# Kernel tuning notes

Hardware: AMD Instinct MI355X
Metric: run time of the kernel (lower is better)

The kernel has to match this reference:

```python
import jax, jax.numpy as jnp
import numpy as np

H = 16        # num_heads
D_HEAD = 128  # head_dim
D = H * D_HEAD  # hidden_size = 2048


def setup_inputs() -> dict:
    key = jax.random.key(0)
    ks = jax.random.split(key, 9)
    s = 1.0 / np.sqrt(D)
    x = jax.random.normal(ks[0], (2, 2048, D), dtype=jnp.float32)
    Wq = jax.random.uniform(ks[1], (D, D), jnp.float32, -s, s)
    bq = jax.random.uniform(ks[2], (D,), jnp.float32, -s, s)
    Wk = jax.random.uniform(ks[3], (D, D), jnp.float32, -s, s)
    bk = jax.random.uniform(ks[4], (D,), jnp.float32, -s, s)
    Wv = jax.random.uniform(ks[5], (D, D), jnp.float32, -s, s)
    bv = jax.random.uniform(ks[6], (D,), jnp.float32, -s, s)
    Wo = jax.random.uniform(ks[7], (D, D), jnp.float32, -s, s)
    bo = jax.random.uniform(ks[8], (D,), jnp.float32, -s, s)
    return {"x": x, "Wq": Wq, "bq": bq, "Wk": Wk, "bk": bk,
            "Wv": Wv, "bv": bv, "Wo": Wo, "bo": bo}


def reference(x, Wq, bq, Wk, bk, Wv, bv, Wo, bo):
    B, T, _ = x.shape
    # Linear projections (torch Linear: x @ W.T + b)
    Q = x @ Wq.T + bq
    K = x @ Wk.T + bk
    V = x @ Wv.T + bv
    # [B, T, H, Dh] -> [B, H, T, Dh]
    Q = Q.reshape(B, T, H, D_HEAD).transpose(0, 2, 1, 3)
    K = K.reshape(B, T, H, D_HEAD).transpose(0, 2, 1, 3)
    V = V.reshape(B, T, H, D_HEAD).transpose(0, 2, 1, 3)
    scores = jnp.einsum('bhqd,bhkd->bhqk', Q, K) / jnp.sqrt(jnp.float32(D_HEAD))
    causal = jnp.tril(jnp.ones((T, T), dtype=bool))
    scores = jnp.where(causal, scores, -jnp.inf)
    probs = jax.nn.softmax(scores, axis=-1)
    ctx = jnp.einsum('bhqk,bhkd->bhqd', probs, V)  # [B, H, T, Dh]
    merged = ctx.transpose(0, 2, 1, 3).reshape(B, T, D)
    return merged @ Wo.T + bo
```

## Files before the change

### kernel.cpp

```cpp
#include <hip/hip_runtime.h>
#include <hip/hip_bf16.h>
#include <math.h>

typedef unsigned short ushort_t;
typedef short bf16x8 __attribute__((ext_vector_type(8)));
typedef float f32x4 __attribute__((ext_vector_type(4)));
typedef float f32x16 __attribute__((ext_vector_type(16)));

#define NH 16
#define DH 128
#define DM 2048
#define TSEQ 2048
#define BT 4096

__device__ __forceinline__ void async16(const void* g, void* l) {
  __builtin_amdgcn_global_load_lds(
      (const __attribute__((address_space(1))) void*)g,
      (__attribute__((address_space(3))) void*)l, 16, 0, 0);
}

__device__ __forceinline__ f32x4 mfma16(bf16x8 a, bf16x8 b, f32x4 c) {
  return __builtin_amdgcn_mfma_f32_16x16x32_bf16(a, b, c, 0, 0, 0);
}
__device__ __forceinline__ f32x16 mfma32(bf16x8 a, bf16x8 b, f32x16 c) {
  return __builtin_amdgcn_mfma_f32_32x32x16_bf16(a, b, c, 0, 0, 0);
}

__device__ __forceinline__ ushort_t f2bf(float f) {
  __hip_bfloat16 h = __float2bfloat16(f);
  return *reinterpret_cast<ushort_t*>(&h);
}
__device__ __forceinline__ unsigned cvtpk_bf16(float lo, float hi_) {
  unsigned r;
  asm("v_cvt_pk_bf16_f32 %0, %1, %2" : "=v"(r) : "v"(lo), "v"(hi_));
  return r;
}
__device__ __forceinline__ float fexp2(float x) {
  float r; asm("v_exp_f32 %0, %1" : "=v"(r) : "v"(x)); return r;
}

__global__ void cvt_all_kernel(const float* __restrict__ x,
                               const float* __restrict__ Wq, const float* __restrict__ Wk,
                               const float* __restrict__ Wv, const float* __restrict__ Wo,
                               ushort_t* __restrict__ xb,
                               ushort_t* __restrict__ Wqb, ushort_t* __restrict__ Wkb,
                               ushort_t* __restrict__ Wvb, ushort_t* __restrict__ Wob)
{
  const int i = blockIdx.x * blockDim.x + threadIdx.x;
  const float* src; ushort_t* dst; int off;
  if (i < (1 << 21)) {
    src = x; dst = xb; off = i;
  } else {
    const int j = i - (1 << 21);
    const int w = j >> 20;
    off = j & ((1 << 20) - 1);
    src = (w == 0) ? Wq : (w == 1) ? Wk : (w == 2) ? Wv : Wo;
    dst = (w == 0) ? Wqb : (w == 1) ? Wkb : (w == 2) ? Wvb : Wob;
  }
  const float4 v = reinterpret_cast<const float4*>(src)[off];
  ushort4 u;
  u.x = f2bf(v.x); u.y = f2bf(v.y); u.z = f2bf(v.z); u.w = f2bf(v.w);
  reinterpret_cast<ushort4*>(dst)[off] = u;
}

__device__ __forceinline__ void stage_half_g(const ushort_t* __restrict__ src,
                                             int row0, int k0,
                                             ushort_t* dst, int tid) {
#pragma unroll
  for (int i = 0; i < 2; ++i) {
    const int idx = i * 512 + tid;
    const int r = idx >> 3, ch = idx & 7;
    const int c = (ch ^ (r & 7)) * 8;
    async16(src + (size_t)(row0 + r) * DM + k0 + c, dst + idx * 8);
  }
}

__global__ __launch_bounds__(512, 2)
void gemm_qkv_fused(const ushort_t* __restrict__ A,
                    const ushort_t* __restrict__ W_0, const ushort_t* __restrict__ W_1,
                    const ushort_t* __restrict__ W_2,
                    const float* __restrict__ b_0, const float* __restrict__ b_1,
                    const float* __restrict__ b_2,
                    ushort_t* __restrict__ outQ, ushort_t* __restrict__ outK,
                    ushort_t* __restrict__ outVt)
{
  constexpr int NK = DM / 64;
  __shared__ __attribute__((aligned(16))) ushort_t As[2][128 * 64];
  __shared__ __attribute__((aligned(16))) ushort_t Bs[2][3][128 * 64];

  const int n0 = blockIdx.x * 128;
  const int m0 = blockIdx.y * 128;
  const int tid = threadIdx.x;
  const int w = tid >> 6, l = tid & 63;
  const int wr = w >> 2, wc = w & 3;
  const int l15 = l & 15, l4 = l >> 4;

  f32x4 acc[3][4][2] = {};
  bf16x8 afr[4][2], bfr[2][2];

  stage_half_g(A,   m0, 0, As[0],    tid);
  stage_half_g(W_0, n0, 0, Bs[0][0], tid);
  stage_half_g(W_1, n0, 0, Bs[0][1], tid);
  stage_half_g(W_2, n0, 0, Bs[0][2], tid);

  for (int kt = 0; kt < NK; ++kt) {
    const int cur = kt & 1;
    if (kt + 1 < NK) {
      const int k1 = (kt + 1) * 64;
      stage_half_g(A,   m0, k1, As[cur ^ 1],    tid);
      stage_half_g(W_0, n0, k1, Bs[cur ^ 1][0], tid);
      stage_half_g(W_1, n0, k1, Bs[cur ^ 1][1], tid);
      stage_half_g(W_2, n0, k1, Bs[cur ^ 1][2], tid);
      asm volatile("s_waitcnt vmcnt(8)" ::: "memory");
    } else {
      asm volatile("s_waitcnt vmcnt(0)" ::: "memory");
    }
    __builtin_amdgcn_s_barrier();

    {
      const char* p_ = reinterpret_cast<const char*>(As[cur]);
#pragma unroll
      for (int mf = 0; mf < 4; ++mf) {
        const int row_ = wr * 64 + mf * 16 + l15;
#pragma unroll
        for (int ks = 0; ks < 2; ++ks)
          afr[mf][ks] = *reinterpret_cast<const bf16x8*>(
              p_ + row_ * 128 + ((l4 * 16 + ks * 64) ^ ((row_ & 7) << 4)));
      }
    }
#pragma unroll
    for (int z = 0; z < 3; ++z) {
      const char* p_ = reinterpret_cast<const char*>(Bs[cur][z]);
#pragma unroll
      for (int nf = 0; nf < 2; ++nf) {
        const int row_ = wc * 32 + nf * 16 + l15;
#pragma unroll
        for (int ks = 0; ks < 2; ++ks)
          bfr[nf][ks] = *reinterpret_cast<const bf16x8*>(
              p_ + row_ * 128 + ((l4 * 16 + ks * 64) ^ ((row_ & 7) << 4)));
      }
      __builtin_amdgcn_s_setprio(1);
#pragma unroll
      for (int mf = 0; mf < 4; ++mf)
#pragma unroll
        for (int nf = 0; nf < 2; ++nf)
#pragma unroll
          for (int ks = 0; ks < 2; ++ks)
            acc[z][mf][nf] = mfma16(afr[mf][ks], bfr[nf][ks], acc[z][mf][nf]);
      __builtin_amdgcn_s_setprio(0);
    }
    asm volatile("" ::: "memory");
    __builtin_amdgcn_s_barrier();
  }

#pragma unroll
  for (int z = 0; z < 3; ++z) {
    const float* bias = (z == 0) ? b_0 : (z == 1) ? b_1 : b_2;
#pragma unroll
    for (int nf = 0; nf < 2; ++nf) {
      const int n = n0 + wc * 32 + nf * 16 + l15;
      const float bv = bias[n];
      const int hh = n >> 7, d = n & 127;
#pragma unroll
      for (int mf = 0; mf < 4; ++mf) {
#pragma unroll
        for (int r = 0; r < 4; ++r) {
          const int m = m0 + wr * 64 + mf * 16 + l4 * 4 + r;
          const float v = acc[z][mf][nf][r] + bv;
          const int b = m >> 11, t = m & 2047;
          const ushort_t val = f2bf(v);
          if (z == 2) {
            outVt[((size_t)(b * NH + hh) * DH + d) * TSEQ + t] = val;
          } else {
            ushort_t* dst = (z == 0) ? outQ : outK;
            dst[((size_t)(b * NH + hh) * TSEQ + t) * DH + d] = val;
          }
        }
      }
    }
  }
}

__device__ __forceinline__ void stage_ab(const ushort_t* __restrict__ A,
                                         const ushort_t* __restrict__ Wp,
                                         int m0, int n0, int k0,
                                         ushort_t* AsB, ushort_t* BsB,
                                         int w, int l)
{
#pragma unroll
  for (int i = 0; i < 4; ++i) {
    const int rb = (i * 4 + w) * 8;
    const int r = rb + (l >> 3);
    const int c = ((l & 7) * 8) ^ ((r & 7) * 8);
    async16(A  + (size_t)(m0 + r) * DM + k0 + c, AsB + rb * 64);
    async16(Wp + (size_t)(n0 + r) * DM + k0 + c, BsB + rb * 64);
  }
}

__global__ __launch_bounds__(256)
void gemm_proj_kernel(const ushort_t* __restrict__ A, const ushort_t* __restrict__ W_0,
                      const float* __restrict__ b_0, float* __restrict__ outF)
{
  constexpr int NK = DM / 64;
  __shared__ __attribute__((aligned(16))) ushort_t As[2][128 * 64];
  __shared__ __attribute__((aligned(16))) ushort_t Bs[2][128 * 64];

  const int n0 = blockIdx.x * 128;
  const int m0 = blockIdx.y * 128;
  const int tid = threadIdx.x;
  const int w = tid >> 6, l = tid & 63;
  const int wm = w >> 1, wn = w & 1;
  const int l15 = l & 15, l4 = l >> 4;

  f32x4 zero = {0.f, 0.f, 0.f, 0.f};
  f32x4 acc[4][4];
#pragma unroll
  for (int i = 0; i < 4; ++i)
#pragma unroll
    for (int j = 0; j < 4; ++j) acc[i][j] = zero;

  stage_ab(A, W_0, m0, n0, 0, As[0], Bs[0], w, l);

  for (int kt = 0; kt < NK; ++kt) {
    const int cur = kt & 1;
    if (kt + 1 < NK) {
      stage_ab(A, W_0, m0, n0, (kt + 1) * 64, As[cur ^ 1], Bs[cur ^ 1], w, l);
      asm volatile("s_waitcnt vmcnt(8)" ::: "memory");
    } else {
      asm volatile("s_waitcnt vmcnt(0)" ::: "memory");
    }
    __builtin_amdgcn_s_barrier();

#pragma unroll
    for (int ks = 0; ks < 2; ++ks) {
      bf16x8 af[4], bfr[4];
#pragma unroll
      for (int mf = 0; mf < 4; ++mf) {
        const int row = wm * 64 + mf * 16 + l15;
        const int byte_ = row * 128 + ((l4 * 16 + ks * 64) ^ ((row & 7) << 4));
        af[mf] = *reinterpret_cast<const bf16x8*>(reinterpret_cast<const char*>(As[cur]) + byte_);
      }
#pragma unroll
      for (int nf = 0; nf < 4; ++nf) {
        const int row = wn * 64 + nf * 16 + l15;
        const int byte_ = row * 128 + ((l4 * 16 + ks * 64) ^ ((row & 7) << 4));
        bfr[nf] = *reinterpret_cast<const bf16x8*>(reinterpret_cast<const char*>(Bs[cur]) + byte_);
      }
      __builtin_amdgcn_s_setprio(1);
#pragma unroll
      for (int mf = 0; mf < 4; ++mf)
#pragma unroll
        for (int nf = 0; nf < 4; ++nf)
          acc[mf][nf] = mfma16(af[mf], bfr[nf], acc[mf][nf]);
      __builtin_amdgcn_s_setprio(0);
    }
    asm volatile("" ::: "memory");
    __builtin_amdgcn_s_barrier();
  }

#pragma unroll
  for (int nf = 0; nf < 4; ++nf) {
    const int n = n0 + wn * 64 + nf * 16 + l15;
    const float bv = b_0[n];
#pragma unroll
    for (int mf = 0; mf < 4; ++mf) {
#pragma unroll
      for (int r = 0; r < 4; ++r) {
        const int m = m0 + wm * 64 + mf * 16 + l4 * 4 + r;
        outF[(size_t)m * DM + n] = acc[mf][nf][r] + bv;
      }
    }
  }
}

__device__ __forceinline__ void stage_kv(const ushort_t* __restrict__ Kg,
                                         const ushort_t* __restrict__ Vt,
                                         size_t kbase, size_t vbase, int kv0,
                                         ushort_t* KsB, ushort_t* VsB, int tid)
{
#pragma unroll
  for (int i = 0; i < 4; ++i) {
    const int idx = i * 256 + tid;
    const int r = idx >> 4, ch = idx & 15;
    const int c = (ch ^ (r & 7)) * 8;
    async16(Kg + kbase + (size_t)(kv0 + r) * DH + c, KsB + idx * 8);
  }
#pragma unroll
  for (int i = 0; i < 4; ++i) {
    const int idx = i * 256 + tid;
    const int d = idx >> 3, ch = idx & 7;
    const int c = (ch ^ (d & 7)) * 8;
    async16(Vt + vbase + (size_t)d * TSEQ + kv0 + c, VsB + idx * 8);
  }
}

__global__ __launch_bounds__(256)
void attn_kernel(const ushort_t* __restrict__ Q, const ushort_t* __restrict__ Kg,
                 const ushort_t* __restrict__ Vt, ushort_t* __restrict__ ctx)
{
  __shared__ __attribute__((aligned(16))) ushort_t Ks[2][64 * 128];
  __shared__ __attribute__((aligned(16))) ushort_t Vs[2][128 * 64];

  const int fid = (int)blockIdx.x + 16 * (int)blockIdx.y;
  const int xcd = fid & 7;
  const int s   = fid >> 3;
  const int bh  = xcd * 4 + (s & 3);
  const int qt  = (s < 32) ? (15 - (s >> 2)) : ((s - 32) >> 2);

  const int tid = threadIdx.x, w = tid >> 6, l = tid & 63;
  const int l31 = l & 31, hi = l >> 5;
  const size_t kbase = (size_t)bh * TSEQ * DH;
  const size_t vbase = (size_t)bh * DH * TSEQ;
  const int bq0 = qt * 128;
  const int wq0 = bq0 + w * 32;
  const int NT = qt * 2 + 2;
  const int q = wq0 + l31;
  const float C2 = 0.12753842f;
  const float NEG = -3.0e38f;

  bf16x8 aq[8];
  {
    const ushort_t* qp = Q + kbase + (size_t)q * DH + hi * 8;
#pragma unroll
    for (int st = 0; st < 8; ++st)
      aq[st] = *reinterpret_cast<const bf16x8*>(qp + st * 16);
  }

  f32x16 o[4] = {};
  float m_r = NEG, l_r = 0.f;

  stage_kv(Kg, Vt, kbase, vbase, 0, Ks[0], Vs[0], tid);

  for (int kt = 0; kt < NT; ++kt) {
    const int kv0 = kt * 64, cur = kt & 1;
    if (kt + 1 < NT) {
      stage_kv(Kg, Vt, kbase, vbase, kv0 + 64, Ks[cur ^ 1], Vs[cur ^ 1], tid);
      asm volatile("s_waitcnt vmcnt(8)" ::: "memory");
    } else {
      asm volatile("s_waitcnt vmcnt(0)" ::: "memory");
    }
    __builtin_amdgcn_s_barrier();

    if (kv0 <= wq0 + 31) {
      const char* ksb = reinterpret_cast<const char*>(Ks[cur]);
      f32x16 s0 = {}, s1 = {};
      __builtin_amdgcn_s_setprio(1);
#pragma unroll
      for (int st = 0; st < 8; ++st) {
        const int byt = l31 * 256 + ((hi * 16 + st * 32) ^ ((l31 & 7) << 4));
        bf16x8 ak0 = *reinterpret_cast<const bf16x8*>(ksb + byt);
        bf16x8 ak1 = *reinterpret_cast<const bf16x8*>(ksb + byt + 8192);
        s0 = mfma32(ak0, aq[st], s0);
        s1 = mfma32(ak1, aq[st], s1);
      }
      __builtin_amdgcn_s_setprio(0);

      if (kv0 + 63 > wq0) {
#pragma unroll
        for (int r = 0; r < 16; ++r) {
          const int kvl = kv0 + (r & 3) + 8 * (r >> 2) + 4 * hi;
          if (kvl > q)      s0[r] = NEG;
          if (kvl + 32 > q) s1[r] = NEG;
        }
      }

      float t8[8];
#pragma unroll
      for (int r = 0; r < 8; ++r)
        t8[r] = fmaxf(fmaxf(s0[r], s0[r + 8]), fmaxf(s1[r], s1[r + 8]));
#pragma unroll
      for (int r = 0; r < 4; ++r) t8[r] = fmaxf(t8[r], t8[r + 4]);
      float mt = fmaxf(fmaxf(t8[0], t8[1]), fmaxf(t8[2], t8[3]));
      mt = fmaxf(mt, __shfl_xor(mt, 32));

      const float mnew = fmaxf(m_r, mt);
      if (!__all(mt <= m_r + 16.0f)) {
        const float alpha = fexp2((m_r - mnew) * C2);
        l_r *= alpha;
#pragma unroll
        for (int d0 = 0; d0 < 4; ++d0) o[d0] *= alpha;
        m_r = mnew;
      }

#pragma unroll
      for (int r = 0; r < 16; ++r) {
        s0[r] = fexp2((s0[r] - m_r) * C2);
        s1[r] = fexp2((s1[r] - m_r) * C2);
      }
      float sm[8];
#pragma unroll
      for (int r = 0; r < 8; ++r) sm[r] = (s0[r] + s0[r + 8]) + (s1[r] + s1[r + 8]);
#pragma unroll
      for (int r = 0; r < 4; ++r) sm[r] += sm[r + 4];
      float ls = (sm[0] + sm[1]) + (sm[2] + sm[3]);
      ls += __shfl_xor(ls, 32);
      l_r += ls;

      const char* vsb = reinterpret_cast<const char*>(Vs[cur]);
#pragma unroll
      for (int ks = 0; ks < 4; ++ks) {
        float pj[8];
#pragma unroll
        for (int j = 0; j < 8; ++j)
          pj[j] = (ks >> 1) ? s1[(ks & 1) * 8 + j] : s0[(ks & 1) * 8 + j];
        unsigned cA = cvtpk_bf16(pj[0], pj[1]);
        unsigned cB = cvtpk_bf16(pj[2], pj[3]);
        unsigned cC = cvtpk_bf16(pj[4], pj[5]);
        unsigned cD = cvtpk_bf16(pj[6], pj[7]);
        asm volatile("v_permlane32_swap_b32 %0, %1" : "+v"(cA), "+v"(cC));
        asm volatile("v_permlane32_swap_b32 %0, %1" : "+v"(cB), "+v"(cD));
        union { unsigned u[4]; bf16x8 v; } pa;
        pa.u[0] = cA; pa.u[1] = cB; pa.u[2] = cC; pa.u[3] = cD;
        __builtin_amdgcn_s_setprio(1);
#pragma unroll
        for (int d0 = 0; d0 < 4; ++d0) {
          const int byt = (d0 * 32 + l31) * 128 + ((ks * 32 + hi * 16) ^ ((l31 & 7) << 4));
          bf16x8 av = *reinterpret_cast<const bf16x8*>(vsb + byt);
          o[d0] = mfma32(av, pa.v, o[d0]);
        }
        __builtin_amdgcn_s_setprio(0);
      }
    }
    asm volatile("" ::: "memory");
    __builtin_amdgcn_s_barrier();
  }

  const size_t obase = (size_t)(bh >> 4) * TSEQ * DM + (size_t)(bh & 15) * DH;
  const float inv = 1.0f / l_r;
  ushort_t* cp = ctx + obase + (size_t)q * DM + hi * 4;
#pragma unroll
  for (int d0 = 0; d0 < 4; ++d0) {
#pragma unroll
    for (int g = 0; g < 4; ++g) {
      ushort4 u;
      u.x = f2bf(o[d0][4 * g + 0] * inv);
      u.y = f2bf(o[d0][4 * g + 1] * inv);
      u.z = f2bf(o[d0][4 * g + 2] * inv);
      u.w = f2bf(o[d0][4 * g + 3] * inv);
      *reinterpret_cast<ushort4*>(cp + d0 * 32 + 8 * g) = u;
    }
  }
}

extern "C" void kernel_launch(void* const* d_in, const int* in_sizes, int n_in,
                              void* d_out, int out_size, void* d_ws, size_t ws_size,
                              hipStream_t stream) {
  const float* x  = (const float*)d_in[0];
  const float* Wq = (const float*)d_in[1];
  const float* bq = (const float*)d_in[2];
  const float* Wk = (const float*)d_in[3];
  const float* bk = (const float*)d_in[4];
  const float* Wv = (const float*)d_in[5];
  const float* bv = (const float*)d_in[6];
  const float* Wo = (const float*)d_in[7];
  const float* bo = (const float*)d_in[8];
  float* out = (float*)d_out;

  char* ws = (char*)d_ws;
  ushort_t* xb  = (ushort_t*)ws;  ws += (size_t)BT * DM * 2;
  ushort_t* Wqb = (ushort_t*)ws;  ws += (size_t)DM * DM * 2;
  ushort_t* Wkb = (ushort_t*)ws;  ws += (size_t)DM * DM * 2;
  ushort_t* Wvb = (ushort_t*)ws;  ws += (size_t)DM * DM * 2;
  ushort_t* Wob = (ushort_t*)ws;  ws += (size_t)DM * DM * 2;
  ushort_t* Qb  = (ushort_t*)ws;  ws += (size_t)BT * DM * 2;
  ushort_t* Kb  = (ushort_t*)ws;  ws += (size_t)BT * DM * 2;
  ushort_t* Vtb = (ushort_t*)ws;  ws += (size_t)BT * DM * 2;
  ushort_t* ctxb = xb;

  cvt_all_kernel<<<6 * (1 << 20) / 256, 256, 0, stream>>>(
      x, Wq, Wk, Wv, Wo, xb, Wqb, Wkb, Wvb, Wob);

  gemm_qkv_fused<<<dim3(16, 32), 512, 0, stream>>>(
      xb, Wqb, Wkb, Wvb, bq, bk, bv, Qb, Kb, Vtb);

  attn_kernel<<<dim3(TSEQ / 128, 32), 256, 0, stream>>>(Qb, Kb, Vtb, ctxb);

  gemm_proj_kernel<<<dim3(16, 32), 256, 0, stream>>>(ctxb, Wob, bo, out);
}
```

Measured before the change: 271.9 us.

## Use single barrier per iteration with wait after compute in all pipelined loops

Restructures the double-buffered loops in the QKV GEMM, output GEMM and attention kernels so each iteration issues the next tile's async loads, computes on the current buffer, then waits for all loads and hits one barrier. This replaces the previous scheme of a partial vmcnt wait plus two barriers per iteration. It removes a barrier per iteration and lets loads overlap the whole compute phase, but the full vmcnt(0) wait happens only at iteration end, so load latency is hidden only if compute is long enough.

Result: no change. 271.5 us, median of 2 (-0.2%).

```diff
diff --git a/kernel.cpp b/kernel.cpp
--- a/kernel.cpp
+++ b/kernel.cpp
@@ -38,6 +38,10 @@
 __device__ __forceinline__ float fexp2(float x) {
   float r; asm("v_exp_f32 %0, %1" : "=v"(r) : "v"(x)); return r;
 }
+
+#define VM0()  asm volatile("s_waitcnt vmcnt(0)" ::: "memory")
+#define BARR() { asm volatile("" ::: "memory"); __builtin_amdgcn_s_barrier(); \
+                 asm volatile("" ::: "memory"); }
 
 __global__ void cvt_all_kernel(const float* __restrict__ x,
                                const float* __restrict__ Wq, const float* __restrict__ Wk,
@@ -102,20 +106,19 @@
   stage_half_g(W_0, n0, 0, Bs[0][0], tid);
   stage_half_g(W_1, n0, 0, Bs[0][1], tid);
   stage_half_g(W_2, n0, 0, Bs[0][2], tid);
+  VM0();
+  BARR();
 
   for (int kt = 0; kt < NK; ++kt) {
     const int cur = kt & 1;
-    if (kt + 1 < NK) {
+    const bool more = (kt + 1 < NK);
+    if (more) {
       const int k1 = (kt + 1) * 64;
       stage_half_g(A,   m0, k1, As[cur ^ 1],    tid);
       stage_half_g(W_0, n0, k1, Bs[cur ^ 1][0], tid);
       stage_half_g(W_1, n0, k1, Bs[cur ^ 1][1], tid);
       stage_half_g(W_2, n0, k1, Bs[cur ^ 1][2], tid);
-      asm volatile("s_waitcnt vmcnt(8)" ::: "memory");
-    } else {
-      asm volatile("s_waitcnt vmcnt(0)" ::: "memory");
-    }
-    __builtin_amdgcn_s_barrier();
+    }
 
     {
       const char* p_ = reinterpret_cast<const char*>(As[cur]);
@@ -149,8 +152,9 @@
             acc[z][mf][nf] = mfma16(afr[mf][ks], bfr[nf][ks], acc[z][mf][nf]);
       __builtin_amdgcn_s_setprio(0);
     }
-    asm volatile("" ::: "memory");
-    __builtin_amdgcn_s_barrier();
+
+    if (more) { VM0(); }
+    BARR();
   }
 
 #pragma unroll
@@ -220,16 +224,14 @@
     for (int j = 0; j < 4; ++j) acc[i][j] = zero;
 
   stage_ab(A, W_0, m0, n0, 0, As[0], Bs[0], w, l);
+  VM0();
+  BARR();
 
   for (int kt = 0; kt < NK; ++kt) {
     const int cur = kt & 1;
-    if (kt + 1 < NK) {
+    const bool more = (kt + 1 < NK);
+    if (more)
       stage_ab(A, W_0, m0, n0, (kt + 1) * 64, As[cur ^ 1], Bs[cur ^ 1], w, l);
-      asm volatile("s_waitcnt vmcnt(8)" ::: "memory");
-    } else {
-      asm volatile("s_waitcnt vmcnt(0)" ::: "memory");
-    }
-    __builtin_amdgcn_s_barrier();
 
 #pragma unroll
     for (int ks = 0; ks < 2; ++ks) {
@@ -254,8 +256,9 @@
           acc[mf][nf] = mfma16(af[mf], bfr[nf], acc[mf][nf]);
       __builtin_amdgcn_s_setprio(0);
     }
-    asm volatile("" ::: "memory");
-    __builtin_amdgcn_s_barrier();
+
+    if (more) { VM0(); }
+    BARR();
   }
 
 #pragma unroll
@@ -330,16 +333,14 @@
   float m_r = NEG, l_r = 0.f;
 
   stage_kv(Kg, Vt, kbase, vbase, 0, Ks[0], Vs[0], tid);
+  VM0();
+  BARR();
 
   for (int kt = 0; kt < NT; ++kt) {
     const int kv0 = kt * 64, cur = kt & 1;
-    if (kt + 1 < NT) {
+    const bool more = (kt + 1 < NT);
+    if (more)
       stage_kv(Kg, Vt, kbase, vbase, kv0 + 64, Ks[cur ^ 1], Vs[cur ^ 1], tid);
-      asm volatile("s_waitcnt vmcnt(8)" ::: "memory");
-    } else {
-      asm volatile("s_waitcnt vmcnt(0)" ::: "memory");
-    }
-    __builtin_amdgcn_s_barrier();
 
     if (kv0 <= wq0 + 31) {
       const char* ksb = reinterpret_cast<const char*>(Ks[cur]);
@@ -421,8 +422,9 @@
         __builtin_amdgcn_s_setprio(0);
       }
     }
-    asm volatile("" ::: "memory");
-    __builtin_amdgcn_s_barrier();
+
+    if (more) { VM0(); }
+    BARR();
   }
 
   const size_t obase = (size_t)(bh >> 4) * TSEQ * DM + (size_t)(bh & 15) * DH;
```
